# Optimization experiments

Hardware: AMD Instinct MI355X
Metric: run time of the kernel (lower is better)

Reference implementation:

```python
import jax, jax.numpy as jnp
import numpy as np

B, S, D = 4, 2048, 2048
NH, NKV = 16, 4
HD = D // NH  # 128


def setup_inputs() -> dict:
    key = jax.random.key(0)
    ks = jax.random.split(key, 6)
    sd = 1.0 / np.sqrt(D)
    return {
        "x": jax.random.normal(ks[0], (B, S, D), jnp.float32),
        "cos": jax.random.normal(ks[1], (1, 1, S, HD), jnp.float32),
        "sin": jax.random.normal(ks[2], (1, 1, S, HD), jnp.float32),
        "wq_w": jax.random.normal(ks[3], (D, D), jnp.float32) * sd,
        "wk_w": jax.random.normal(ks[4], (NKV * HD, D), jnp.float32) * sd,
        "wv_w": jax.random.normal(ks[5], (NKV * HD, D), jnp.float32) * sd,
        "start_pos": 0,
    }


def _rotate_half(t):
    h = t.shape[-1] // 2
    return jnp.concatenate([-t[..., h:], t[..., :h]], axis=-1)


def reference(x, cos, sin, wq_w, wk_w, wv_w, start_pos):
    b, s, d = x.shape
    n_rep = NH // NKV
    q = (x @ wq_w.T).reshape(b, s, NH, HD).transpose(0, 2, 1, 3)      # [b,H,s,hd]
    k = (x @ wk_w.T).reshape(b, s, NKV, HD).transpose(0, 2, 1, 3)     # [b,Hk,s,hd]
    v = (x @ wv_w.T).reshape(b, s, NKV, HD).transpose(0, 2, 1, 3)
    # rotary
    q = q * cos + _rotate_half(q) * sin
    k = k * cos + _rotate_half(k) * sin
    # repeat_kv
    k = jnp.repeat(k, n_rep, axis=1)   # [b,H,s,hd]
    v = jnp.repeat(v, n_rep, axis=1)
    scores = jnp.einsum("bhqd,bhkd->bhqk", q, k) / jnp.sqrt(jnp.float32(HD))
    causal = jnp.tril(jnp.ones((s, s), dtype=bool))
    scores = jnp.where(causal, scores, jnp.float32(-jnp.inf))
    w = jax.nn.softmax(scores, axis=-1)
    out = jnp.einsum("bhqk,bhkd->bhqd", w, v)
    return out.transpose(0, 2, 1, 3).reshape(b, s, d)
```

## Files before the change

### kernel.cpp

```cpp
#include <hip/hip_runtime.h>
#include <hip/hip_bf16.h>
#include <math.h>

#define B_ 4
#define S_ 2048
#define D_ 2048
#define NH_ 16
#define NKV_ 4
#define HD_ 128

typedef short bf16x8 __attribute__((ext_vector_type(8)));
typedef float f32x4 __attribute__((ext_vector_type(4)));
typedef unsigned u32x4 __attribute__((ext_vector_type(4)));
typedef __hip_bfloat16 bf16;

#define ASYNC_CP16(gp, lp)                                                    \
  __builtin_amdgcn_global_load_lds(                                           \
      (const __attribute__((address_space(1))) unsigned int*)(gp),            \
      (__attribute__((address_space(3))) unsigned int*)(lp), 16, 0, 0)

__global__ __launch_bounds__(256) void cvt_kernel(const float* __restrict__ in,
                                                  bf16* __restrict__ out, int n4) {
  int i = blockIdx.x * 256 + threadIdx.x;
  if (i >= n4) return;
  float4 v = ((const float4*)in)[i];
  union { ushort4 u; bf16 h[4]; } o;
  o.h[0] = __float2bfloat16(v.x);
  o.h[1] = __float2bfloat16(v.y);
  o.h[2] = __float2bfloat16(v.z);
  o.h[3] = __float2bfloat16(v.w);
  ((ushort4*)out)[i] = o.u;
}

__global__ __launch_bounds__(256) void gemm_qkv(
    const bf16* __restrict__ A, const bf16* __restrict__ W,
    bf16* __restrict__ qr, bf16* __restrict__ kr, bf16* __restrict__ vlin,
    const float* __restrict__ cosp, const float* __restrict__ sinp,
    float qscale) {
  __shared__ __align__(16) bf16 As[128 * 64];
  __shared__ __align__(16) bf16 Bs[128 * 64];
  const int tid = threadIdx.x;
  const int lane = tid & 63, wave = tid >> 6;
  const int wm = (wave & 1) * 64, wn = (wave >> 1) * 64;
  const int m0 = blockIdx.x * 128;
  const int hblk = blockIdx.y;
  const int n0 = hblk * 128;
  const int quad = lane >> 4, c = lane & 15;
  const int K = 2048;

  f32x4 acc[4][4] = {};

  const int sr = lane >> 3;
  const int sg = lane & 7;
  const int gc = (sg ^ sr) * 8;
  const bf16* Ap = A + (size_t)(m0 + wave * 32 + sr) * K + gc;
  const bf16* Bp = W + (size_t)(n0 + wave * 32 + sr) * K + gc;

  for (int kb = 0; kb < K; kb += 64) {
    __syncthreads();
#pragma unroll
    for (int i = 0; i < 4; i++) {
      ASYNC_CP16(Ap + (size_t)(i * 8) * K + kb, &As[(wave * 32 + i * 8) * 64]);
      ASYNC_CP16(Bp + (size_t)(i * 8) * K + kb, &Bs[(wave * 32 + i * 8) * 64]);
    }
    __syncthreads();
#pragma unroll
    for (int kk = 0; kk < 2; kk++) {
      const int slot = ((kk * 4 + quad) ^ (c & 7)) * 8;
      bf16x8 af[4], bfr[4];
#pragma unroll
      for (int t = 0; t < 4; t++) {
        af[t]  = *(const bf16x8*)(&As[(wm + t * 16 + c) * 64 + slot]);
        bfr[t] = *(const bf16x8*)(&Bs[(wn + t * 16 + c) * 64 + slot]);
      }
#pragma unroll
      for (int mt = 0; mt < 4; mt++)
#pragma unroll
        for (int nt = 0; nt < 4; nt++)
          acc[mt][nt] = __builtin_amdgcn_mfma_f32_16x16x32_bf16(
              af[mt], bfr[nt], acc[mt][nt], 0, 0, 0);
    }
  }

  if (hblk >= 20) {
    const int colb = (hblk - 20) * 128 + wn;
#pragma unroll
    for (int mt = 0; mt < 4; mt++)
#pragma unroll
      for (int reg = 0; reg < 4; reg++) {
        int m = m0 + wm + mt * 16 + quad * 4 + reg;
        bf16* row = vlin + (size_t)m * (NKV_ * HD_) + colb;
#pragma unroll
        for (int nt = 0; nt < 4; nt++)
          row[nt * 16 + c] = __float2bfloat16(acc[mt][nt][reg]);
      }
  } else {
    float* Sc = (float*)As;
    __syncthreads();
    if (wave >= 2) {
#pragma unroll
      for (int mt = 0; mt < 4; mt++)
#pragma unroll
        for (int reg = 0; reg < 4; reg++) {
          int lr = wm + mt * 16 + quad * 4 + reg;
#pragma unroll
          for (int nt = 0; nt < 4; nt++)
            Sc[lr * 64 + nt * 16 + c] = acc[mt][nt][reg];
        }
    }
    __syncthreads();
    if (wave < 2) {
      const float scale = (hblk < 16) ? qscale : 1.0f;
#pragma unroll
      for (int mt = 0; mt < 4; mt++)
#pragma unroll
        for (int reg = 0; reg < 4; reg++) {
          int lr = wm + mt * 16 + quad * 4 + reg;
          int m = m0 + lr;
          int b = m >> 11, s = m & 2047;
          const float* cr = cosp + s * HD_;
          const float* sn = sinp + s * HD_;
          bf16* orow = (hblk < 16)
              ? qr + ((size_t)(b * NH_ + hblk) * S_ + s) * HD_
              : kr + ((size_t)(b * NKV_ + (hblk - 16)) * S_ + s) * HD_;
#pragma unroll
          for (int nt = 0; nt < 4; nt++) {
            int d1 = nt * 16 + c, d2 = d1 + 64;
            float q1 = acc[mt][nt][reg];
            float q2 = Sc[lr * 64 + d1];
            float o1 = (q1 * cr[d1] - q2 * sn[d1]) * scale;
            float o2 = (q2 * cr[d2] + q1 * sn[d2]) * scale;
            orow[d1] = __float2bfloat16(o1);
            orow[d2] = __float2bfloat16(o2);
          }
        }
    }
  }
}

__global__ __launch_bounds__(256) void v_transpose(const bf16* __restrict__ in,
                                                   int instride,
                                                   bf16* __restrict__ out) {
  __shared__ __align__(16) bf16 tile[64][HD_ + 8];
  int bidx = blockIdx.x;
  int st = bidx & 31;
  int kv = (bidx >> 5) & 3;
  int b = bidx >> 7;
  int s0 = st * 64;
  int t = threadIdx.x;
  {
    int row = t >> 2;
    int colb = (t & 3) * 32;
#pragma unroll
    for (int i = 0; i < 4; i++) {
      int col = colb + i * 8;
      *(uint4*)(&tile[row][col]) = *(const uint4*)(
          &in[(size_t)(b * S_ + s0 + row) * instride + kv * HD_ + col]);
    }
  }
  __syncthreads();
  int sl = t & 63, hb = t >> 6;
#pragma unroll
  for (int i = 0; i < 32; i++) {
    int hd = i * 4 + hb;
    out[((size_t)(b * NKV_ + kv) * HD_ + hd) * S_ + s0 + sl] = tile[sl][hd];
  }
}

__device__ __forceinline__ void attn_step(
    const bf16* __restrict__ Ks, const bf16* __restrict__ Vs,
    bf16* __restrict__ Psw, const bf16x8* qf, f32x4* o,
    float& m_i, float& l_i, bool diag, int kb, int qbase, int quad, int c) {
  f32x4 sacc[4] = {};
#pragma unroll
  for (int kt = 0; kt < 4; kt++) {
    const int slot = ((kt * 4 + quad) ^ (c & 7)) * 8;
#pragma unroll
    for (int mt = 0; mt < 4; mt++) {
      bf16x8 kf = *(const bf16x8*)(&Ks[(mt * 16 + c) * 128 + slot]);
      sacc[mt] = __builtin_amdgcn_mfma_f32_16x16x32_bf16(kf, qf[kt], sacc[mt], 0, 0, 0);
    }
  }
  if (diag) {
    const int qg = qbase + c;
#pragma unroll
    for (int mt = 0; mt < 4; mt++)
#pragma unroll
      for (int r = 0; r < 4; r++)
        if (kb + mt * 16 + quad * 4 + r > qg) sacc[mt][r] = -INFINITY;
  }
  f32x4 mx4 = __builtin_elementwise_max(
      __builtin_elementwise_max(sacc[0], sacc[1]),
      __builtin_elementwise_max(sacc[2], sacc[3]));
  float mx = fmaxf(fmaxf(mx4[0], mx4[1]), fmaxf(mx4[2], mx4[3]));
  mx = fmaxf(mx, __shfl_xor(mx, 16, 64));
  mx = fmaxf(mx, __shfl_xor(mx, 32, 64));
  const float mnew = fmaxf(m_i, mx);
  const float alpha = exp2f(m_i - mnew);
  m_i = mnew;
  const f32x4 mn4 = {mnew, mnew, mnew, mnew};
  f32x4 rs4 = {0.f, 0.f, 0.f, 0.f};
#pragma unroll
  for (int mt = 0; mt < 4; mt++) {
    f32x4 e = sacc[mt] - mn4;
    f32x4 p;
    p[0] = exp2f(e[0]); p[1] = exp2f(e[1]);
    p[2] = exp2f(e[2]); p[3] = exp2f(e[3]);
    rs4 += p;
    u32x4 u = __builtin_bit_cast(u32x4, p) + 0x8000u;
    uint2 pk;
    pk.x = __builtin_amdgcn_perm(u[1], u[0], 0x07060302u);
    pk.y = __builtin_amdgcn_perm(u[3], u[2], 0x07060302u);
    const int pslot = mt * 2 + (quad >> 1);
    *(uint2*)(&Psw[c * 64 + ((pslot ^ (c & 7)) << 3) + (quad & 1) * 4]) = pk;
  }
  float rs = (rs4[0] + rs4[1]) + (rs4[2] + rs4[3]);
  rs += __shfl_xor(rs, 16, 64);
  rs += __shfl_xor(rs, 32, 64);
  l_i = l_i * alpha + rs;
  if (__any(alpha != 1.0f)) {
    f32x4 av;
    av[0] = __shfl(alpha, quad * 4 + 0, 64);
    av[1] = __shfl(alpha, quad * 4 + 1, 64);
    av[2] = __shfl(alpha, quad * 4 + 2, 64);
    av[3] = __shfl(alpha, quad * 4 + 3, 64);
#pragma unroll
    for (int nt = 0; nt < 8; nt++) o[nt] *= av;
  }
#pragma unroll
  for (int kk = 0; kk < 2; kk++) {
    bf16x8 pf = *(const bf16x8*)(&Psw[c * 64 + (((kk * 4 + quad) ^ (c & 7)) << 3)]);
    const int slot = ((kk * 4 + quad) ^ (c & 7)) * 8;
#pragma unroll
    for (int nt = 0; nt < 8; nt++) {
      bf16x8 vf = *(const bf16x8*)(&Vs[(nt * 16 + c) * 64 + slot]);
      o[nt] = __builtin_amdgcn_mfma_f32_16x16x32_bf16(pf, vf, o[nt], 0, 0, 0);
    }
  }
}

__global__ __launch_bounds__(256, 4) void attn_kernel(const bf16* __restrict__ Q,
                                                      const bf16* __restrict__ Kr,
                                                      const bf16* __restrict__ Vt,
                                                      float* __restrict__ O) {
  __shared__ __align__(16) bf16 Ks[64 * 128];
  __shared__ __align__(16) bf16 Vs[128 * 64];
  __shared__ __align__(16) bf16 Ps[4][16 * 64];

  const int tid = threadIdx.x, lane = tid & 63, wave = tid >> 6;
  const int quad = lane >> 4, c = lane & 15;
  const int j = blockIdx.x;
  const int bh = blockIdx.y;
  const int b = bh >> 4, h = bh & 15, kv = h >> 2;
  bf16* Psw = &Ps[wave][0];

  const bf16* kbase = Kr + (size_t)(b * NKV_ + kv) * S_ * HD_;
  const bf16* vbase = Vt + (size_t)(b * NKV_ + kv) * HD_ * S_;

  int koff[4], voff;
  {
    const int kl = lane >> 4;
    const int ks = lane & 15;
#pragma unroll
    for (int i = 0; i < 4; i++) {
      int r = wave * 16 + i * 4 + kl;
      koff[i] = r * HD_ + ((ks ^ (r & 7)) * 8);
    }
    const int vl = lane >> 3;
    const int vs = lane & 7;
    voff = (wave * 32 + vl) * S_ + ((vs ^ (vl & 7)) * 8);
  }

#pragma unroll 1
  for (int pass = 0; pass < 2; ++pass) {
    const int qt = pass ? (31 - j) : j;
    const int q0 = qt * 64;
    const int qb = q0 + wave * 16;

    bf16x8 qf[4];
    {
      const bf16* qp = Q + ((size_t)(b * NH_ + h) * S_ + qb + c) * HD_;
#pragma unroll
      for (int kt = 0; kt < 4; kt++)
        qf[kt] = *(const bf16x8*)(qp + kt * 32 + quad * 8);
    }
    f32x4 o_acc[8] = {};
    float m_i = -INFINITY, l_i = 0.f;

#pragma unroll 1
    for (int it = 0; it <= qt; ++it) {
      const int kb = it * 64;
      __syncthreads();
#pragma unroll
      for (int i = 0; i < 4; i++) {
        ASYNC_CP16(kbase + (size_t)kb * HD_ + koff[i], &Ks[(wave * 16 + i * 4) * 128]);
        ASYNC_CP16(vbase + kb + voff + (size_t)(i * 8) * S_, &Vs[(wave * 32 + i * 8) * 64]);
      }
      __syncthreads();
      attn_step(Ks, Vs, Psw, qf, o_acc, m_i, l_i, it == qt, kb, qb, quad, c);
    }

    float inv[4];
#pragma unroll
    for (int r = 0; r < 4; r++) inv[r] = 1.0f / __shfl(l_i, quad * 4 + r, 64);
    float* obase = O + (size_t)b * S_ * D_ + (size_t)h * HD_;
#pragma unroll
    for (int nt = 0; nt < 8; nt++)
#pragma unroll
      for (int r = 0; r < 4; r++)
        obase[(size_t)(qb + quad * 4 + r) * D_ + nt * 16 + c] = o_acc[nt][r] * inv[r];
  }
}

extern "C" void kernel_launch(void* const* d_in, const int* in_sizes, int n_in,
                              void* d_out, int out_size, void* d_ws, size_t ws_size,
                              hipStream_t stream) {
  const float* x    = (const float*)d_in[0];
  const float* cosp = (const float*)d_in[1];
  const float* sinp = (const float*)d_in[2];
  const float* wq   = (const float*)d_in[3];
  const float* wk   = (const float*)d_in[4];
  const float* wv   = (const float*)d_in[5];
  float* out = (float*)d_out;

  char* ws = (char*)d_ws;
  const size_t MB = 1024 * 1024;
  bf16* xb    = (bf16*)(ws + 0);
  bf16* wqkvb = (bf16*)(ws + 32 * MB);
  bf16* qr    = (bf16*)(ws + 44 * MB);
  bf16* kr    = (bf16*)(ws + 76 * MB);
  bf16* vlin  = (bf16*)(ws + 84 * MB);
  bf16* vt    = (bf16*)(ws + 92 * MB);

  cvt_kernel<<<16384, 256, 0, stream>>>(x, xb, 4194304);
  cvt_kernel<<<4096, 256, 0, stream>>>(wq, wqkvb, 1048576);
  cvt_kernel<<<1024, 256, 0, stream>>>(wk, wqkvb + 4194304, 262144);
  cvt_kernel<<<1024, 256, 0, stream>>>(wv, wqkvb + 5242880, 262144);

  const float qscale = 1.4426950408889634f / 11.313708498984761f;
  gemm_qkv<<<dim3(64, 24), 256, 0, stream>>>(xb, wqkvb, qr, kr, vlin,
                                             cosp, sinp, qscale);

  v_transpose<<<512, 256, 0, stream>>>(vlin, NKV_ * HD_, vt);

  attn_kernel<<<dim3(16, 64), 256, 0, stream>>>(qr, kr, vt, out);
}
```

Baseline: 386.8 us.

## Double-buffer K/V tiles, lazily rescale softmax, raise priority around MFMAs

The K/V shared-memory tiles become two buffers, so the next tile's async global-to-LDS copy is issued before the current tile is computed, with one barrier per iteration instead of two. The online softmax now only moves the running max, and rescales the accumulator and row sum, when the new max exceeds the old one by more than 8 in log2 units. Otherwise it keeps the stale max, which is safe in fp32. s_setprio is raised around the MFMA loops. The larger LDS footprint (about 72KB per block) likely cuts resident blocks per CU below the launch bound of 4, trading occupancy for overlap.

```diff
diff --git a/kernel.cpp b/kernel.cpp
--- a/kernel.cpp
+++ b/kernel.cpp
@@ -172,6 +172,7 @@
     bf16* __restrict__ Psw, const bf16x8* qf, f32x4* o,
     float& m_i, float& l_i, bool diag, int kb, int qbase, int quad, int c) {
   f32x4 sacc[4] = {};
+  __builtin_amdgcn_s_setprio(1);
 #pragma unroll
   for (int kt = 0; kt < 4; kt++) {
     const int slot = ((kt * 4 + quad) ^ (c & 7)) * 8;
@@ -181,6 +182,7 @@
       sacc[mt] = __builtin_amdgcn_mfma_f32_16x16x32_bf16(kf, qf[kt], sacc[mt], 0, 0, 0);
     }
   }
+  __builtin_amdgcn_s_setprio(0);
   if (diag) {
     const int qg = qbase + c;
 #pragma unroll
@@ -195,10 +197,20 @@
   float mx = fmaxf(fmaxf(mx4[0], mx4[1]), fmaxf(mx4[2], mx4[3]));
   mx = fmaxf(mx, __shfl_xor(mx, 16, 64));
   mx = fmaxf(mx, __shfl_xor(mx, 32, 64));
-  const float mnew = fmaxf(m_i, mx);
-  const float alpha = exp2f(m_i - mnew);
-  m_i = mnew;
-  const f32x4 mn4 = {mnew, mnew, mnew, mnew};
+  if (!__all(mx - m_i <= 8.0f)) {
+    const float mnew = fmaxf(m_i, mx);
+    const float alpha = exp2f(m_i - mnew);
+    m_i = mnew;
+    l_i *= alpha;
+    f32x4 av;
+    av[0] = __shfl(alpha, quad * 4 + 0, 64);
+    av[1] = __shfl(alpha, quad * 4 + 1, 64);
+    av[2] = __shfl(alpha, quad * 4 + 2, 64);
+    av[3] = __shfl(alpha, quad * 4 + 3, 64);
+#pragma unroll
+    for (int nt = 0; nt < 8; nt++) o[nt] *= av;
+  }
+  const f32x4 mn4 = {m_i, m_i, m_i, m_i};
   f32x4 rs4 = {0.f, 0.f, 0.f, 0.f};
 #pragma unroll
   for (int mt = 0; mt < 4; mt++) {
@@ -217,25 +229,18 @@
   float rs = (rs4[0] + rs4[1]) + (rs4[2] + rs4[3]);
   rs += __shfl_xor(rs, 16, 64);
   rs += __shfl_xor(rs, 32, 64);
-  l_i = l_i * alpha + rs;
-  if (__any(alpha != 1.0f)) {
-    f32x4 av;
-    av[0] = __shfl(alpha, quad * 4 + 0, 64);
-    av[1] = __shfl(alpha, quad * 4 + 1, 64);
-    av[2] = __shfl(alpha, quad * 4 + 2, 64);
-    av[3] = __shfl(alpha, quad * 4 + 3, 64);
-#pragma unroll
-    for (int nt = 0; nt < 8; nt++) o[nt] *= av;
-  }
+  l_i += rs;
 #pragma unroll
   for (int kk = 0; kk < 2; kk++) {
     bf16x8 pf = *(const bf16x8*)(&Psw[c * 64 + (((kk * 4 + quad) ^ (c & 7)) << 3)]);
     const int slot = ((kk * 4 + quad) ^ (c & 7)) * 8;
+    __builtin_amdgcn_s_setprio(1);
 #pragma unroll
     for (int nt = 0; nt < 8; nt++) {
       bf16x8 vf = *(const bf16x8*)(&Vs[(nt * 16 + c) * 64 + slot]);
       o[nt] = __builtin_amdgcn_mfma_f32_16x16x32_bf16(pf, vf, o[nt], 0, 0, 0);
     }
+    __builtin_amdgcn_s_setprio(0);
   }
 }
 
@@ -243,8 +248,8 @@
                                                       const bf16* __restrict__ Kr,
                                                       const bf16* __restrict__ Vt,
                                                       float* __restrict__ O) {
-  __shared__ __align__(16) bf16 Ks[64 * 128];
-  __shared__ __align__(16) bf16 Vs[128 * 64];
+  __shared__ __align__(16) bf16 Ks[2][64 * 128];
+  __shared__ __align__(16) bf16 Vs[2][128 * 64];
   __shared__ __align__(16) bf16 Ps[4][16 * 64];
 
   const int tid = threadIdx.x, lane = tid & 63, wave = tid >> 6;
@@ -271,6 +276,17 @@
     voff = (wave * 32 + vl) * S_ + ((vs ^ (vl & 7)) * 8);
   }
 
+#define STAGE(kb_, buf_)                                                      \
+  do {                                                                        \
+    _Pragma("unroll")                                                         \
+    for (int i_ = 0; i_ < 4; i_++) {                                          \
+      ASYNC_CP16(kbase + (size_t)(kb_) * HD_ + koff[i_],                      \
+                 &Ks[buf_][(wave * 16 + i_ * 4) * 128]);                      \
+      ASYNC_CP16(vbase + (kb_) + voff + (size_t)(i_ * 8) * S_,                \
+                 &Vs[buf_][(wave * 32 + i_ * 8) * 64]);                       \
+    }                                                                         \
+  } while (0)
+
 #pragma unroll 1
   for (int pass = 0; pass < 2; ++pass) {
     const int qt = pass ? (31 - j) : j;
@@ -287,17 +303,17 @@
     f32x4 o_acc[8] = {};
     float m_i = -INFINITY, l_i = 0.f;
 
+    __syncthreads();
+    STAGE(0, 0);
+    int cur = 0;
+
 #pragma unroll 1
     for (int it = 0; it <= qt; ++it) {
-      const int kb = it * 64;
       __syncthreads();
-#pragma unroll
-      for (int i = 0; i < 4; i++) {
-        ASYNC_CP16(kbase + (size_t)kb * HD_ + koff[i], &Ks[(wave * 16 + i * 4) * 128]);
-        ASYNC_CP16(vbase + kb + voff + (size_t)(i * 8) * S_, &Vs[(wave * 32 + i * 8) * 64]);
-      }
-      __syncthreads();
-      attn_step(Ks, Vs, Psw, qf, o_acc, m_i, l_i, it == qt, kb, qb, quad, c);
+      if (it < qt) STAGE((it + 1) * 64, cur ^ 1);
+      attn_step(&Ks[cur][0], &Vs[cur][0], Psw, qf, o_acc, m_i, l_i,
+                it == qt, it * 64, qb, quad, c);
+      cur ^= 1;
     }
 
     float inv[4];
@@ -310,6 +326,7 @@
       for (int r = 0; r < 4; r++)
         obase[(size_t)(qb + quad * 4 + r) * D_ + nt * 16 + c] = o_acc[nt][r] * inv[r];
   }
+#undef STAGE
 }
 
 extern "C" void kernel_launch(void* const* d_in, const int* in_sizes, int n_in,
```

After: 412.6 us. +6.7%, slower.

## Process two 16-row query subtiles per wave to reuse K/V fragments

Applied to the files above, without the earlier changes.

Each wave now handles 32 query rows, split into two 16-row subtiles that share every K and V fragment loaded from LDS. This halves LDS reads per MFMA and per unit of output. Each block covers a 128-row query tile instead of pairing two 64-row tiles, and blocks are launched largest-first. The online softmax now skips rescaling unless the running max grows by more than 8 (lazy rescale). In exchange, register use doubles for accumulators, the occupancy hint drops from 4 to 3, and causal work per block becomes less balanced.

```diff
diff --git a/kernel.cpp b/kernel.cpp
--- a/kernel.cpp
+++ b/kernel.cpp
@@ -167,92 +167,117 @@
   }
 }
 
-__device__ __forceinline__ void attn_step(
+__device__ __forceinline__ void attn_step2(
     const bf16* __restrict__ Ks, const bf16* __restrict__ Vs,
-    bf16* __restrict__ Psw, const bf16x8* qf, f32x4* o,
-    float& m_i, float& l_i, bool diag, int kb, int qbase, int quad, int c) {
-  f32x4 sacc[4] = {};
+    bf16* __restrict__ PsA, bf16* __restrict__ PsB,
+    const bf16x8* qfA, const bf16x8* qfB, f32x4* oA, f32x4* oB,
+    float& mA, float& lA, float& mB, float& lB,
+    bool diagA, bool diagB, int kb, int qbA, int quad, int c) {
+  f32x4 sA[4] = {}, sB[4] = {};
 #pragma unroll
   for (int kt = 0; kt < 4; kt++) {
     const int slot = ((kt * 4 + quad) ^ (c & 7)) * 8;
 #pragma unroll
     for (int mt = 0; mt < 4; mt++) {
       bf16x8 kf = *(const bf16x8*)(&Ks[(mt * 16 + c) * 128 + slot]);
-      sacc[mt] = __builtin_amdgcn_mfma_f32_16x16x32_bf16(kf, qf[kt], sacc[mt], 0, 0, 0);
-    }
-  }
-  if (diag) {
-    const int qg = qbase + c;
+      sA[mt] = __builtin_amdgcn_mfma_f32_16x16x32_bf16(kf, qfA[kt], sA[mt], 0, 0, 0);
+      sB[mt] = __builtin_amdgcn_mfma_f32_16x16x32_bf16(kf, qfB[kt], sB[mt], 0, 0, 0);
+    }
+  }
+  if (diagA) {
+    const int qg = qbA + c;
 #pragma unroll
     for (int mt = 0; mt < 4; mt++)
 #pragma unroll
       for (int r = 0; r < 4; r++)
-        if (kb + mt * 16 + quad * 4 + r > qg) sacc[mt][r] = -INFINITY;
-  }
-  f32x4 mx4 = __builtin_elementwise_max(
-      __builtin_elementwise_max(sacc[0], sacc[1]),
-      __builtin_elementwise_max(sacc[2], sacc[3]));
-  float mx = fmaxf(fmaxf(mx4[0], mx4[1]), fmaxf(mx4[2], mx4[3]));
-  mx = fmaxf(mx, __shfl_xor(mx, 16, 64));
-  mx = fmaxf(mx, __shfl_xor(mx, 32, 64));
-  const float mnew = fmaxf(m_i, mx);
-  const float alpha = exp2f(m_i - mnew);
-  m_i = mnew;
-  const f32x4 mn4 = {mnew, mnew, mnew, mnew};
-  f32x4 rs4 = {0.f, 0.f, 0.f, 0.f};
-#pragma unroll
-  for (int mt = 0; mt < 4; mt++) {
-    f32x4 e = sacc[mt] - mn4;
-    f32x4 p;
-    p[0] = exp2f(e[0]); p[1] = exp2f(e[1]);
-    p[2] = exp2f(e[2]); p[3] = exp2f(e[3]);
-    rs4 += p;
-    u32x4 u = __builtin_bit_cast(u32x4, p) + 0x8000u;
-    uint2 pk;
-    pk.x = __builtin_amdgcn_perm(u[1], u[0], 0x07060302u);
-    pk.y = __builtin_amdgcn_perm(u[3], u[2], 0x07060302u);
-    const int pslot = mt * 2 + (quad >> 1);
-    *(uint2*)(&Psw[c * 64 + ((pslot ^ (c & 7)) << 3) + (quad & 1) * 4]) = pk;
-  }
-  float rs = (rs4[0] + rs4[1]) + (rs4[2] + rs4[3]);
-  rs += __shfl_xor(rs, 16, 64);
-  rs += __shfl_xor(rs, 32, 64);
-  l_i = l_i * alpha + rs;
-  if (__any(alpha != 1.0f)) {
-    f32x4 av;
-    av[0] = __shfl(alpha, quad * 4 + 0, 64);
-    av[1] = __shfl(alpha, quad * 4 + 1, 64);
-    av[2] = __shfl(alpha, quad * 4 + 2, 64);
-    av[3] = __shfl(alpha, quad * 4 + 3, 64);
-#pragma unroll
-    for (int nt = 0; nt < 8; nt++) o[nt] *= av;
-  }
+        if (kb + mt * 16 + quad * 4 + r > qg) sA[mt][r] = -INFINITY;
+  }
+  if (diagB) {
+    const int qg = qbA + 16 + c;
+#pragma unroll
+    for (int mt = 0; mt < 4; mt++)
+#pragma unroll
+      for (int r = 0; r < 4; r++)
+        if (kb + mt * 16 + quad * 4 + r > qg) sB[mt][r] = -INFINITY;
+  }
+
+#define SOFTMAX_PACK(sacc, m_i, l_i, o, Psw)                                  \
+  do {                                                                        \
+    f32x4 mx4 = __builtin_elementwise_max(                                    \
+        __builtin_elementwise_max(sacc[0], sacc[1]),                          \
+        __builtin_elementwise_max(sacc[2], sacc[3]));                         \
+    float mx = fmaxf(fmaxf(mx4[0], mx4[1]), fmaxf(mx4[2], mx4[3]));          \
+    mx = fmaxf(mx, __shfl_xor(mx, 16, 64));                                   \
+    mx = fmaxf(mx, __shfl_xor(mx, 32, 64));                                   \
+    if (!__all(mx - m_i <= 8.0f)) {                                           \
+      const float mnew = fmaxf(m_i, mx);                                      \
+      const float alpha = exp2f(m_i - mnew);                                  \
+      m_i = mnew;                                                             \
+      l_i *= alpha;                                                           \
+      f32x4 av;                                                               \
+      av[0] = __shfl(alpha, quad * 4 + 0, 64);                                \
+      av[1] = __shfl(alpha, quad * 4 + 1, 64);                                \
+      av[2] = __shfl(alpha, quad * 4 + 2, 64);                                \
+      av[3] = __shfl(alpha, quad * 4 + 3, 64);                                \
+      _Pragma("unroll")                                                       \
+      for (int nt = 0; nt < 8; nt++) o[nt] *= av;                             \
+    }                                                                         \
+    const f32x4 mn4 = {m_i, m_i, m_i, m_i};                                   \
+    f32x4 rs4 = {0.f, 0.f, 0.f, 0.f};                                         \
+    _Pragma("unroll")                                                         \
+    for (int mt = 0; mt < 4; mt++) {                                          \
+      f32x4 e = sacc[mt] - mn4;                                               \
+      f32x4 p;                                                                \
+      p[0] = exp2f(e[0]); p[1] = exp2f(e[1]);                                 \
+      p[2] = exp2f(e[2]); p[3] = exp2f(e[3]);                                 \
+      rs4 += p;                                                               \
+      u32x4 u = __builtin_bit_cast(u32x4, p) + 0x8000u;                       \
+      uint2 pk;                                                               \
+      pk.x = __builtin_amdgcn_perm(u[1], u[0], 0x07060302u);                  \
+      pk.y = __builtin_amdgcn_perm(u[3], u[2], 0x07060302u);                  \
+      const int pslot = mt * 2 + (quad >> 1);                                 \
+      *(uint2*)(&Psw[c * 64 + ((pslot ^ (c & 7)) << 3) + (quad & 1) * 4]) = pk; \
+    }                                                                         \
+    float rs = (rs4[0] + rs4[1]) + (rs4[2] + rs4[3]);                         \
+    rs += __shfl_xor(rs, 16, 64);                                             \
+    rs += __shfl_xor(rs, 32, 64);                                             \
+    l_i += rs;                                                                \
+  } while (0)
+
+  SOFTMAX_PACK(sA, mA, lA, oA, PsA);
+  SOFTMAX_PACK(sB, mB, lB, oB, PsB);
+#undef SOFTMAX_PACK
+
 #pragma unroll
   for (int kk = 0; kk < 2; kk++) {
-    bf16x8 pf = *(const bf16x8*)(&Psw[c * 64 + (((kk * 4 + quad) ^ (c & 7)) << 3)]);
+    const int psl = (((kk * 4 + quad) ^ (c & 7)) << 3);
+    bf16x8 pfA = *(const bf16x8*)(&PsA[c * 64 + psl]);
+    bf16x8 pfB = *(const bf16x8*)(&PsB[c * 64 + psl]);
     const int slot = ((kk * 4 + quad) ^ (c & 7)) * 8;
 #pragma unroll
     for (int nt = 0; nt < 8; nt++) {
       bf16x8 vf = *(const bf16x8*)(&Vs[(nt * 16 + c) * 64 + slot]);
-      o[nt] = __builtin_amdgcn_mfma_f32_16x16x32_bf16(pf, vf, o[nt], 0, 0, 0);
-    }
-  }
-}
-
-__global__ __launch_bounds__(256, 4) void attn_kernel(const bf16* __restrict__ Q,
+      oA[nt] = __builtin_amdgcn_mfma_f32_16x16x32_bf16(pfA, vf, oA[nt], 0, 0, 0);
+      oB[nt] = __builtin_amdgcn_mfma_f32_16x16x32_bf16(pfB, vf, oB[nt], 0, 0, 0);
+    }
+  }
+}
+
+__global__ __launch_bounds__(256, 3) void attn_kernel(const bf16* __restrict__ Q,
                                                       const bf16* __restrict__ Kr,
                                                       const bf16* __restrict__ Vt,
                                                       float* __restrict__ O) {
   __shared__ __align__(16) bf16 Ks[64 * 128];
   __shared__ __align__(16) bf16 Vs[128 * 64];
-  __shared__ __align__(16) bf16 Ps[4][16 * 64];
+  __shared__ __align__(16) bf16 Ps[4][2][16 * 64];
 
   const int tid = threadIdx.x, lane = tid & 63, wave = tid >> 6;
   const int quad = lane >> 4, c = lane & 15;
-  const int j = blockIdx.x;
+  const int jj = 15 - blockIdx.x;
   const int bh = blockIdx.y;
   const int b = bh >> 4, h = bh & 15, kv = h >> 2;
-  bf16* Psw = &Ps[wave][0];
+  bf16* PsA = &Ps[wave][0][0];
+  bf16* PsB = &Ps[wave][1][0];
 
   const bf16* kbase = Kr + (size_t)(b * NKV_ + kv) * S_ * HD_;
   const bf16* vbase = Vt + (size_t)(b * NKV_ + kv) * HD_ * S_;
@@ -271,44 +296,58 @@
     voff = (wave * 32 + vl) * S_ + ((vs ^ (vl & 7)) * 8);
   }
 
+  const int q0 = jj * 128;
+  const int qb = q0 + wave * 32;
+  const int nsteps = 2 * jj + 2;
+
+  bf16x8 qfA[4], qfB[4];
+  {
+    const bf16* qpA = Q + ((size_t)(b * NH_ + h) * S_ + qb + c) * HD_;
+    const bf16* qpB = qpA + (size_t)16 * HD_;
+#pragma unroll
+    for (int kt = 0; kt < 4; kt++) {
+      qfA[kt] = *(const bf16x8*)(qpA + kt * 32 + quad * 8);
+      qfB[kt] = *(const bf16x8*)(qpB + kt * 32 + quad * 8);
+    }
+  }
+  f32x4 oA[8] = {}, oB[8] = {};
+  float mA = -INFINITY, lA = 0.f, mB = -INFINITY, lB = 0.f;
+
 #pragma unroll 1
-  for (int pass = 0; pass < 2; ++pass) {
-    const int qt = pass ? (31 - j) : j;
-    const int q0 = qt * 64;
-    const int qb = q0 + wave * 16;
-
-    bf16x8 qf[4];
-    {
-      const bf16* qp = Q + ((size_t)(b * NH_ + h) * S_ + qb + c) * HD_;
-#pragma unroll
-      for (int kt = 0; kt < 4; kt++)
-        qf[kt] = *(const bf16x8*)(qp + kt * 32 + quad * 8);
-    }
-    f32x4 o_acc[8] = {};
-    float m_i = -INFINITY, l_i = 0.f;
-
-#pragma unroll 1
-    for (int it = 0; it <= qt; ++it) {
-      const int kb = it * 64;
-      __syncthreads();
-#pragma unroll
-      for (int i = 0; i < 4; i++) {
-        ASYNC_CP16(kbase + (size_t)kb * HD_ + koff[i], &Ks[(wave * 16 + i * 4) * 128]);
-        ASYNC_CP16(vbase + kb + voff + (size_t)(i * 8) * S_, &Vs[(wave * 32 + i * 8) * 64]);
-      }
-      __syncthreads();
-      attn_step(Ks, Vs, Psw, qf, o_acc, m_i, l_i, it == qt, kb, qb, quad, c);
-    }
-
+  for (int it = 0; it < nsteps; ++it) {
+    const int kb = it * 64;
+    __syncthreads();
+#pragma unroll
+    for (int i = 0; i < 4; i++) {
+      ASYNC_CP16(kbase + (size_t)kb * HD_ + koff[i], &Ks[(wave * 16 + i * 4) * 128]);
+      ASYNC_CP16(vbase + kb + voff + (size_t)(i * 8) * S_, &Vs[(wave * 32 + i * 8) * 64]);
+    }
+    __syncthreads();
+    if (kb <= qb + 31)
+      attn_step2(Ks, Vs, PsA, PsB, qfA, qfB, oA, oB, mA, lA, mB, lB,
+                 kb + 63 > qb, kb + 63 > qb + 16, kb, qb, quad, c);
+  }
+
+  float* obase = O + (size_t)b * S_ * D_ + (size_t)h * HD_;
+  {
     float inv[4];
 #pragma unroll
-    for (int r = 0; r < 4; r++) inv[r] = 1.0f / __shfl(l_i, quad * 4 + r, 64);
-    float* obase = O + (size_t)b * S_ * D_ + (size_t)h * HD_;
+    for (int r = 0; r < 4; r++) inv[r] = 1.0f / __shfl(lA, quad * 4 + r, 64);
 #pragma unroll
     for (int nt = 0; nt < 8; nt++)
 #pragma unroll
       for (int r = 0; r < 4; r++)
-        obase[(size_t)(qb + quad * 4 + r) * D_ + nt * 16 + c] = o_acc[nt][r] * inv[r];
+        obase[(size_t)(qb + quad * 4 + r) * D_ + nt * 16 + c] = oA[nt][r] * inv[r];
+  }
+  {
+    float inv[4];
+#pragma unroll
+    for (int r = 0; r < 4; r++) inv[r] = 1.0f / __shfl(lB, quad * 4 + r, 64);
+#pragma unroll
+    for (int nt = 0; nt < 8; nt++)
+#pragma unroll
+      for (int r = 0; r < 4; r++)
+        obase[(size_t)(qb + 16 + quad * 4 + r) * D_ + nt * 16 + c] = oB[nt][r] * inv[r];
   }
 }
 
```

Result: slower. 527.5 us (+36.4%).
